# Kernel optimization log

Hardware: AMD Instinct MI355X
Metric: run time of the kernel (lower is better)

## Reference

```python
import jax, jax.numpy as jnp
import numpy as np

B, S, D, H = 4, 1024, 1024, 16
DH = D // H  # head dim = 64
PAD = -1e7   # padding_num in source
EPS = 1e-3   # keras LayerNormalization default epsilon


def setup_inputs() -> dict:
    key = jax.random.key(0)
    ks = jax.random.split(key, 8)
    return {
        "queries": jax.random.normal(ks[0], (B, S, D), jnp.float32),
        "keys": jax.random.normal(ks[1], (B, S, D), jnp.float32),
        "values": jax.random.normal(ks[2], (B, S, D), jnp.float32),
        "query_masks": jax.random.randint(ks[3], (B, S), 0, 2, jnp.int32),
        "key_masks": jax.random.randint(ks[4], (B, S), 0, 2, jnp.int32),
        "Wq": jax.random.normal(ks[5], (D, D), jnp.float32) * (D ** -0.5),
        "Wk": jax.random.normal(ks[6], (D, D), jnp.float32) * (D ** -0.5),
        "Wv": jax.random.normal(ks[7], (D, D), jnp.float32) * (D ** -0.5),
        "gamma": jnp.ones((D,), jnp.float32),
        "beta": jnp.zeros((D,), jnp.float32),
    }


def reference(queries, keys, values, query_masks, key_masks, Wq, Wk, Wv, gamma, beta):
    # QKV projections (no bias)
    Q = queries @ Wq  # [B,S,D]
    K = keys @ Wk
    V = values @ Wv
    # split heads: tf.split(axis=2)+concat(axis=0) == head-major layout [H,B,S,DH]
    Qh = Q.reshape(B, S, H, DH).transpose(2, 0, 1, 3)
    Kh = K.reshape(B, S, H, DH).transpose(2, 0, 1, 3)
    Vh = V.reshape(B, S, H, DH).transpose(2, 0, 1, 3)
    # scaled scores; note source scales by head_dim ** 0.5 (d_k of split K)
    scores = jnp.einsum("hbqd,hbkd->hbqk", Qh, Kh) / (DH ** 0.5)
    # additive key mask: positions where key_mask==0 get large negative
    scores = jnp.where(key_masks[None, :, None, :] == 0, PAD, scores)
    attn = jax.nn.softmax(scores, axis=-1)
    # multiplicative query mask AFTER softmax (as in source)
    attn = attn * query_masks[None, :, :, None].astype(jnp.float32)
    out = jnp.einsum("hbqk,hbkd->hbqd", attn, Vh)  # [H,B,S,DH]
    # merge heads back: concat over feature axis in head order
    out = out.transpose(1, 2, 0, 3).reshape(B, S, D)
    # residual + LayerNorm
    res = queries + out
    mean = jnp.mean(res, axis=-1, keepdims=True)
    var = jnp.mean(jnp.square(res - mean), axis=-1, keepdims=True)
    return gamma * (res - mean) * jax.lax.rsqrt(var + EPS) + beta
```

## Files before the change

### kernel.cpp

```cpp
#include <hip/hip_runtime.h>

#define BB   4
#define SS   1024
#define DD   1024
#define HH   16
#define DHH  64
#define LN_EPS  (1e-3f)

typedef unsigned short u16;
typedef __attribute__((ext_vector_type(8))) short bf16x8;
typedef __attribute__((ext_vector_type(4))) float f32x4;

__device__ __forceinline__ u16 f2bf(float f) {
    union { float f; unsigned int u; } v; v.f = f;
    return (u16)((v.u + 0x7FFFu + ((v.u >> 16) & 1u)) >> 16);
}

__device__ __forceinline__ unsigned int cvt_pk_bf16(float lo, float hi) {
    unsigned int r;
    asm("v_cvt_pk_bf16_f32 %0, %1, %2" : "=v"(r) : "v"(lo), "v"(hi));
    return r;
}

__device__ __forceinline__ void cp16(void* lds, const void* g) {
    __builtin_amdgcn_global_load_lds(
        (const __attribute__((address_space(1))) unsigned int*)g,
        (__attribute__((address_space(3))) unsigned int*)lds, 16, 0, 0);
}

__global__ __launch_bounds__(256) void prep(const float* __restrict__ q,
                                            const float* __restrict__ k,
                                            const float* __restrict__ v,
                                            const float* __restrict__ Wq,
                                            const float* __restrict__ Wk,
                                            const float* __restrict__ Wv,
                                            u16* __restrict__ Abf,
                                            u16* __restrict__ WtA) {
    __shared__ float Ts[64][65];
    const int z = blockIdx.z;
    const int tid = threadIdx.x;
    if (z < 3) {
        const float* src = (z == 0) ? q : (z == 1) ? k : v;
        u16* dst = Abf + (size_t)z * ((size_t)BB * SS * DD);
        const int N8 = BB * SS * DD / 8;
        for (int i = blockIdx.x * 256 + tid; i < N8; i += 256 * 256) {
            const float4 f0 = ((const float4*)src)[i * 2];
            const float4 f1 = ((const float4*)src)[i * 2 + 1];
            union { u16 u[8]; uint4 o; } t;
            t.u[0] = f2bf(f0.x); t.u[1] = f2bf(f0.y);
            t.u[2] = f2bf(f0.z); t.u[3] = f2bf(f0.w);
            t.u[4] = f2bf(f1.x); t.u[5] = f2bf(f1.y);
            t.u[6] = f2bf(f1.z); t.u[7] = f2bf(f1.w);
            ((uint4*)dst)[i] = t.o;
        }
    } else {
        const float* W = (z == 3) ? Wq : (z == 4) ? Wk : Wv;
        u16* Wt = WtA + (size_t)(z - 3) * DD * DD;
        const int k0 = (blockIdx.x >> 4) * 64, n0 = (blockIdx.x & 15) * 64;
        #pragma unroll
        for (int it = 0; it < 4; ++it) {
            const int idx = tid + it * 256;
            const int r = idx >> 4, c4 = (idx & 15) * 4;
            const float4 vv = *(const float4*)&W[(size_t)(k0 + r) * DD + n0 + c4];
            Ts[r][c4 + 0] = vv.x; Ts[r][c4 + 1] = vv.y;
            Ts[r][c4 + 2] = vv.z; Ts[r][c4 + 3] = vv.w;
        }
        __syncthreads();
        const int n = tid >> 2, kc = (tid & 3) * 16;
        #pragma unroll
        for (int p = 0; p < 8; ++p) {
            const unsigned int lo = f2bf(Ts[kc + p * 2 + 0][n]);
            const unsigned int hi = f2bf(Ts[kc + p * 2 + 1][n]);
            *(unsigned int*)&Wt[(size_t)(n0 + n) * DD + k0 + kc + p * 2] = lo | (hi << 16);
        }
    }
}

__global__ __launch_bounds__(512, 2) void gemm_fused(const u16* __restrict__ Abf,
                                                     const u16* __restrict__ WtA,
                                                     u16* __restrict__ Qbf,
                                                     u16* __restrict__ Kbf,
                                                     u16* __restrict__ Vtb) {
    __shared__ u16 lds[2][2][2][8192];

    const int bid = blockIdx.x;
    const int swz = (bid & 7) * 24 + (bid >> 3);
    const int z   = swz >> 6;
    const int rem = swz & 63;
    const int m0  = (rem >> 2) * 256;
    const int n0  = (rem & 3) * 256;

    const u16* A  = Abf + (size_t)z * ((size_t)BB * SS * DD);
    const u16* Bm = WtA + (size_t)z * (DD * DD);

    const int tid  = threadIdx.x;
    const int wave = tid >> 6, lane = tid & 63;
    const int ln = lane & 15, quad = lane >> 4;
    const int wr = wave >> 2, wc = wave & 3;

    int r_[2], c_[2];
    #pragma unroll
    for (int rd = 0; rd < 2; ++rd) {
        const int l = rd * 512 + tid;
        const int rr = l >> 2, cs = l & 3;
        r_[rd] = rr;
        c_[rd] = cs ^ ((rr >> 1) & 3);
    }
    const u16* srcA[2] = { A  + (size_t)(m0 + r_[0]) * DD + c_[0] * 8,
                           A  + (size_t)(m0 + r_[1]) * DD + c_[1] * 8 };
    const u16* srcB[2] = { Bm + (size_t)(n0 + r_[0]) * DD + c_[0] * 8,
                           Bm + (size_t)(n0 + r_[1]) * DD + c_[1] * 8 };

    int offA[8], offB[4];
    #pragma unroll
    for (int mi = 0; mi < 8; ++mi) {
        const int r = wr * 128 + mi * 16 + ln;
        offA[mi] = (r * 4 + (quad ^ ((r >> 1) & 3))) * 8;
    }
    #pragma unroll
    for (int nj = 0; nj < 4; ++nj) {
        const int r = wc * 64 + nj * 16 + ln;
        offB[nj] = (r * 4 + (quad ^ ((r >> 1) & 3))) * 8;
    }

    auto stage = [&](int T, int x) {
        const int cb = T & 1;
        const int koff = T * 64 + x * 32;
        #pragma unroll
        for (int rd = 0; rd < 2; ++rd) {
            cp16(&lds[cb][x][0][(rd * 512 + wave * 64) * 8], srcA[rd] + koff);
            cp16(&lds[cb][x][1][(rd * 512 + wave * 64) * 8], srcB[rd] + koff);
        }
    };

    f32x4 acc[8][4] = {};

    stage(0, 0); stage(0, 1); stage(1, 0);
    asm volatile("s_waitcnt vmcnt(8)" ::: "memory");
    __builtin_amdgcn_s_barrier();

    #pragma unroll
    for (int t = 0; t < 16; ++t) {
        const int c = t & 1;
        #pragma unroll
        for (int x = 0; x < 2; ++x) {
            if (x == 0) { if (t < 15) stage(t + 1, 1); }
            else        { if (t < 14) stage(t + 2, 0); }

            bf16x8 af[8], bfv[4];
            const u16* Ar = &lds[c][x][0][0];
            const u16* Br = &lds[c][x][1][0];
            #pragma unroll
            for (int mi = 0; mi < 8; ++mi) af[mi] = *(const bf16x8*)&Ar[offA[mi]];
            #pragma unroll
            for (int nj = 0; nj < 4; ++nj) bfv[nj] = *(const bf16x8*)&Br[offB[nj]];

            if (x == 0) {
                if (t < 15) asm volatile("s_waitcnt vmcnt(8)" ::: "memory");
                else        asm volatile("s_waitcnt vmcnt(0)" ::: "memory");
            } else {
                if (t < 14)       asm volatile("s_waitcnt vmcnt(8)" ::: "memory");
                else if (t == 14) asm volatile("s_waitcnt vmcnt(4)" ::: "memory");
            }
            __builtin_amdgcn_s_barrier();

            __builtin_amdgcn_s_setprio(1);
            #pragma unroll
            for (int mi = 0; mi < 8; ++mi)
                #pragma unroll
                for (int nj = 0; nj < 4; ++nj)
                    acc[mi][nj] = __builtin_amdgcn_mfma_f32_16x16x32_bf16(
                        af[mi], bfv[nj], acc[mi][nj], 0, 0, 0);
            __builtin_amdgcn_s_setprio(0);
            __builtin_amdgcn_s_barrier();
        }
    }

    const int hh = (n0 >> 6) + wc;
    if (z < 2) {
        u16* C = (z == 0) ? Qbf : Kbf;
        const float scale = (z == 0) ? 0.18033688f : 1.0f;
        #pragma unroll
        for (int mi = 0; mi < 8; ++mi) {
            const int mbase = m0 + wr * 128 + mi * 16 + quad * 4;
            const int bb = mbase >> 10, sb = mbase & 1023;
            #pragma unroll
            for (int nj = 0; nj < 4; ++nj) {
                const int dh = nj * 16 + ln;
                #pragma unroll
                for (int r = 0; r < 4; ++r)
                    C[(((size_t)bb * HH + hh) * SS + sb + r) * DHH + dh] =
                        f2bf(acc[mi][nj][r] * scale);
            }
        }
    } else {
        #pragma unroll
        for (int mi = 0; mi < 8; ++mi) {
            const int mbase = m0 + wr * 128 + mi * 16 + quad * 4;
            const int bb = mbase >> 10, sb = mbase & 1023;
            #pragma unroll
            for (int nj = 0; nj < 4; ++nj) {
                const int dh = nj * 16 + ln;
                uint2 pk;
                pk.x = cvt_pk_bf16(acc[mi][nj][0], acc[mi][nj][1]);
                pk.y = cvt_pk_bf16(acc[mi][nj][2], acc[mi][nj][3]);
                *(uint2*)&Vtb[(((size_t)bb * HH + hh) * DHH + dh) * SS + sb] = pk;
            }
        }
    }
}

__global__ __launch_bounds__(512) void attn_mfma(const u16* __restrict__ Qg,
                                                 const u16* __restrict__ Kg,
                                                 const u16* __restrict__ Vtg,
                                                 const int* __restrict__ qmask,
                                                 const int* __restrict__ kmask,
                                                 float* __restrict__ O) {
    __shared__ u16 Ps[128 * 68];
    __shared__ u16 Ks[2][64 * 64];
    __shared__ u16 Vs[2][64 * 64];
    __shared__ float kmLds[SS];

    const int bid  = blockIdx.x;
    const int xcd  = bid & 7;
    const int rest = bid >> 3;
    const int bh   = (rest & 7) * 8 + xcd;
    const int qt   = rest >> 3;
    const int b    = bh >> 4, h = bh & 15;
    const int q0   = qt * 128;
    const int tid  = threadIdx.x;
    const int wave = tid >> 6, lane = tid & 63;
    const int ln = lane & 15, quad = lane >> 4;
    const size_t bhs = (size_t)b * HH + h;

    const int sr = tid >> 3, scsrc = (tid & 7) ^ ((tid >> 3) & 7);
    const u16* kSrc = &Kg[(bhs * SS + sr) * DHH + scsrc * 8];
    const u16* vSrc = &Vtg[(bhs * DHH + sr) * SS + scsrc * 8];
    auto stageKV = [&](int t) {
        const int cb = t & 1;
        cp16(&Ks[cb][wave * 512], kSrc + (size_t)t * 64 * DHH);
        cp16(&Vs[cb][wave * 512], vSrc + t * 64);
    };

    const u16* qrow = &Qg[(bhs * SS + q0 + wave * 16 + ln) * DHH];
    const bf16x8 qf0 = *(const bf16x8*)&qrow[quad * 8];
    const bf16x8 qf1 = *(const bf16x8*)&qrow[32 + quad * 8];
    asm volatile("" ::: "memory");
    if (wave < 4)
        cp16(&kmLds[wave * 256], &kmask[b * SS + (wave * 64 + lane) * 4]);
    stageKV(0);
    stageKV(1);
    asm volatile("s_waitcnt vmcnt(2)" ::: "memory");
    __builtin_amdgcn_s_barrier();

    {
        const int2 iv = *(const int2*)&kmLds[tid * 2];
        float2 fv; fv.x = (float)iv.x; fv.y = (float)iv.y;
        *(float2*)&kmLds[tid * 2] = fv;
    }
    asm volatile("s_waitcnt lgkmcnt(0)" ::: "memory");
    __builtin_amdgcn_s_barrier();

    int off[4][2];
    #pragma unroll
    for (int nt = 0; nt < 4; ++nt) {
        const int r = nt * 16 + ln;
        off[nt][0] = ((r << 3) + ((0 + quad) ^ (r & 7))) << 3;
        off[nt][1] = ((r << 3) + ((4 + quad) ^ (r & 7))) << 3;
    }

    f32x4 o[4] = {};
    float lsum = 0.f;
    const f32x4 zero = {0.f, 0.f, 0.f, 0.f};
    const int prow = (wave * 16 + ln) * 68;

    #pragma unroll 2
    for (int kt = 0; kt < SS / 64; ++kt) {
        const int cb = kt & 1;
        const u16* Kc = Ks[cb];
        const u16* Vc = Vs[cb];

        #pragma unroll
        for (int nt = 0; nt < 4; ++nt) {
            const bf16x8 k0f = *(const bf16x8*)&Kc[off[nt][0]];
            const bf16x8 k1f = *(const bf16x8*)&Kc[off[nt][1]];
            f32x4 sacc = __builtin_amdgcn_mfma_f32_16x16x32_bf16(k0f, qf0, zero, 0, 0, 0);
            sacc = __builtin_amdgcn_mfma_f32_16x16x32_bf16(k1f, qf1, sacc, 0, 0, 0);
            const float4 fm = *(const float4*)&kmLds[kt * 64 + nt * 16 + quad * 4];
            const float p0 = fm.x * __builtin_amdgcn_exp2f(sacc[0]);
            const float p1 = fm.y * __builtin_amdgcn_exp2f(sacc[1]);
            const float p2 = fm.z * __builtin_amdgcn_exp2f(sacc[2]);
            const float p3 = fm.w * __builtin_amdgcn_exp2f(sacc[3]);
            lsum += (p0 + p1) + (p2 + p3);
            uint2 pk;
            pk.x = cvt_pk_bf16(p0, p1);
            pk.y = cvt_pk_bf16(p2, p3);
            *(uint2*)&Ps[prow + nt * 16 + quad * 4] = pk;
        }

        __builtin_amdgcn_s_setprio(1);
        #pragma unroll
        for (int kk2 = 0; kk2 < 2; ++kk2) {
            const bf16x8 pf = *(const bf16x8*)&Ps[prow + kk2 * 32 + quad * 8];
            #pragma unroll
            for (int nt2 = 0; nt2 < 4; ++nt2) {
                const bf16x8 vf = *(const bf16x8*)&Vc[off[nt2][kk2]];
                o[nt2] = __builtin_amdgcn_mfma_f32_16x16x32_bf16(pf, vf, o[nt2], 0, 0, 0);
            }
        }
        __builtin_amdgcn_s_setprio(0);

        if (kt == SS / 64 - 1) break;
        __builtin_amdgcn_s_barrier();
        if (kt + 2 < SS / 64) {
            stageKV(kt + 2);
            asm volatile("s_waitcnt vmcnt(2)" ::: "memory");
        } else {
            asm volatile("s_waitcnt vmcnt(0)" ::: "memory");
        }
        __builtin_amdgcn_s_barrier();
    }

    lsum += __shfl_xor(lsum, 16);
    lsum += __shfl_xor(lsum, 32);
    #pragma unroll
    for (int r = 0; r < 4; ++r) {
        const int qloc = quad * 4 + r;
        const float l = __shfl(lsum, qloc);
        const int q = q0 + wave * 16 + qloc;
        const float scale = (float)qmask[b * SS + q] / l;
        #pragma unroll
        for (int nt2 = 0; nt2 < 4; ++nt2)
            O[((size_t)b * SS + q) * DD + h * DHH + nt2 * 16 + ln] = o[nt2][r] * scale;
    }
}

__global__ __launch_bounds__(256) void ln_kernel(const float* __restrict__ Qin,
                                                 const float* __restrict__ attn,
                                                 const float* __restrict__ gamma,
                                                 const float* __restrict__ beta,
                                                 float* __restrict__ out) {
    const int row = blockIdx.x;
    const int tid = threadIdx.x;
    const int wid = tid >> 6, lane = tid & 63;
    __shared__ float sred[4];

    const float4 qv = ((const float4*)Qin)[(size_t)row * 256 + tid];
    const float4 av = ((const float4*)attn)[(size_t)row * 256 + tid];
    float4 v;
    v.x = qv.x + av.x; v.y = qv.y + av.y;
    v.z = qv.z + av.z; v.w = qv.w + av.w;

    float sum = v.x + v.y + v.z + v.w;
    #pragma unroll
    for (int off = 32; off; off >>= 1) sum += __shfl_down(sum, off);
    if (lane == 0) sred[wid] = sum;
    __syncthreads();
    const float mean = (sred[0] + sred[1] + sred[2] + sred[3]) * (1.0f / DD);
    __syncthreads();

    const float dx = v.x - mean, dy = v.y - mean, dz = v.z - mean, dw = v.w - mean;
    float vs = dx * dx + dy * dy + dz * dz + dw * dw;
    #pragma unroll
    for (int off = 32; off; off >>= 1) vs += __shfl_down(vs, off);
    if (lane == 0) sred[wid] = vs;
    __syncthreads();
    const float var = (sred[0] + sred[1] + sred[2] + sred[3]) * (1.0f / DD);
    const float inv = rsqrtf(var + LN_EPS);

    const float4 g = ((const float4*)gamma)[tid];
    const float4 bt = ((const float4*)beta)[tid];
    float4 ov;
    ov.x = g.x * dx * inv + bt.x; ov.y = g.y * dy * inv + bt.y;
    ov.z = g.z * dz * inv + bt.z; ov.w = g.w * dw * inv + bt.w;
    ((float4*)out)[(size_t)row * 256 + tid] = ov;
}

extern "C" void kernel_launch(void* const* d_in, const int* in_sizes, int n_in,
                              void* d_out, int out_size, void* d_ws, size_t ws_size,
                              hipStream_t stream) {
    const float* queries = (const float*)d_in[0];
    const float* keys    = (const float*)d_in[1];
    const float* values  = (const float*)d_in[2];
    const int*   qmask   = (const int*)d_in[3];
    const int*   kmask   = (const int*)d_in[4];
    const float* Wq      = (const float*)d_in[5];
    const float* Wk      = (const float*)d_in[6];
    const float* Wv      = (const float*)d_in[7];
    const float* gamma   = (const float*)d_in[8];
    const float* beta    = (const float*)d_in[9];
    float* out = (float*)d_out;

    const size_t NTOK = (size_t)BB * SS;
    u16* Abf = (u16*)d_ws;
    float* Ob = (float*)d_ws;
    u16* Qbf = Abf + 3 * NTOK * DD;
    u16* Kbf = Qbf + NTOK * DD;
    u16* Vtb = Kbf + NTOK * DD;
    u16* WtA = Vtb + NTOK * DD;

    prep<<<dim3(256, 1, 6), 256, 0, stream>>>(queries, keys, values, Wq, Wk, Wv, Abf, WtA);

    gemm_fused<<<192, 512, 0, stream>>>(Abf, WtA, Qbf, Kbf, Vtb);

    attn_mfma<<<BB * HH * (SS / 128), 512, 0, stream>>>(Qbf, Kbf, Vtb, qmask, kmask, Ob);

    ln_kernel<<<BB * SS, 256, 0, stream>>>(queries, Ob, gamma, beta, out);
}
```

Baseline: 186.9 us.

## Shrink QKV GEMM tiles to 128x128 with 256-thread blocks and simpler pipeline

Result: no change. 185.2 us (-0.9%).

```diff
diff --git a/kernel.cpp b/kernel.cpp
--- a/kernel.cpp
+++ b/kernel.cpp
@@ -76,19 +76,20 @@
     }
 }
 
-__global__ __launch_bounds__(512, 2) void gemm_fused(const u16* __restrict__ Abf,
-                                                     const u16* __restrict__ WtA,
-                                                     u16* __restrict__ Qbf,
-                                                     u16* __restrict__ Kbf,
-                                                     u16* __restrict__ Vtb) {
-    __shared__ u16 lds[2][2][2][8192];
+__global__ __launch_bounds__(256) void gemm_fused(const u16* __restrict__ Abf,
+                                                  const u16* __restrict__ WtA,
+                                                  u16* __restrict__ Qbf,
+                                                  u16* __restrict__ Kbf,
+                                                  u16* __restrict__ Vtb) {
+    __shared__ u16 As[2][128 * 64];
+    __shared__ u16 Bs[2][128 * 64];
 
     const int bid = blockIdx.x;
-    const int swz = (bid & 7) * 24 + (bid >> 3);
-    const int z   = swz >> 6;
-    const int rem = swz & 63;
-    const int m0  = (rem >> 2) * 256;
-    const int n0  = (rem & 3) * 256;
+    const int swz = (bid & 7) * 96 + (bid >> 3);
+    const int z   = swz >> 8;
+    const int rem = swz & 255;
+    const int m0  = (rem >> 3) * 128;
+    const int n0  = (rem & 7) * 128;
 
     const u16* A  = Abf + (size_t)z * ((size_t)BB * SS * DD);
     const u16* Bm = WtA + (size_t)z * (DD * DD);
@@ -96,114 +97,94 @@
     const int tid  = threadIdx.x;
     const int wave = tid >> 6, lane = tid & 63;
     const int ln = lane & 15, quad = lane >> 4;
-    const int wr = wave >> 2, wc = wave & 3;
-
-    int r_[2], c_[2];
-    #pragma unroll
-    for (int rd = 0; rd < 2; ++rd) {
-        const int l = rd * 512 + tid;
-        const int rr = l >> 2, cs = l & 3;
-        r_[rd] = rr;
-        c_[rd] = cs ^ ((rr >> 1) & 3);
-    }
-    const u16* srcA[2] = { A  + (size_t)(m0 + r_[0]) * DD + c_[0] * 8,
-                           A  + (size_t)(m0 + r_[1]) * DD + c_[1] * 8 };
-    const u16* srcB[2] = { Bm + (size_t)(n0 + r_[0]) * DD + c_[0] * 8,
-                           Bm + (size_t)(n0 + r_[1]) * DD + c_[1] * 8 };
-
-    int offA[8], offB[4];
-    #pragma unroll
-    for (int mi = 0; mi < 8; ++mi) {
-        const int r = wr * 128 + mi * 16 + ln;
-        offA[mi] = (r * 4 + (quad ^ ((r >> 1) & 3))) * 8;
-    }
-    #pragma unroll
-    for (int nj = 0; nj < 4; ++nj) {
-        const int r = wc * 64 + nj * 16 + ln;
-        offB[nj] = (r * 4 + (quad ^ ((r >> 1) & 3))) * 8;
-    }
-
-    auto stage = [&](int T, int x) {
+    const int mw = (wave & 1) * 64, nw = (wave >> 1) * 64;
+
+    const u16* srcA[4];
+    const u16* srcB[4];
+    #pragma unroll
+    for (int w = 0; w < 4; ++w) {
+        const int l = w * 256 + tid;
+        const int r = l >> 3, cs = l & 7;
+        const int c = cs ^ (r & 7);
+        srcA[w] = A  + (size_t)(m0 + r) * DD + c * 8;
+        srcB[w] = Bm + (size_t)(n0 + r) * DD + c * 8;
+    }
+
+    auto stage = [&](int T) {
         const int cb = T & 1;
-        const int koff = T * 64 + x * 32;
-        #pragma unroll
-        for (int rd = 0; rd < 2; ++rd) {
-            cp16(&lds[cb][x][0][(rd * 512 + wave * 64) * 8], srcA[rd] + koff);
-            cp16(&lds[cb][x][1][(rd * 512 + wave * 64) * 8], srcB[rd] + koff);
-        }
+        const int koff = T * 64;
+        #pragma unroll
+        for (int w = 0; w < 4; ++w)
+            cp16(&As[cb][(w * 256 + wave * 64) * 8], srcA[w] + koff);
+        #pragma unroll
+        for (int w = 0; w < 4; ++w)
+            cp16(&Bs[cb][(w * 256 + wave * 64) * 8], srcB[w] + koff);
     };
 
-    f32x4 acc[8][4] = {};
-
-    stage(0, 0); stage(0, 1); stage(1, 0);
-    asm volatile("s_waitcnt vmcnt(8)" ::: "memory");
-    __builtin_amdgcn_s_barrier();
-
+    f32x4 acc[4][4] = {};
+
+    stage(0);
     #pragma unroll
     for (int t = 0; t < 16; ++t) {
-        const int c = t & 1;
-        #pragma unroll
-        for (int x = 0; x < 2; ++x) {
-            if (x == 0) { if (t < 15) stage(t + 1, 1); }
-            else        { if (t < 14) stage(t + 2, 0); }
-
-            bf16x8 af[8], bfv[4];
-            const u16* Ar = &lds[c][x][0][0];
-            const u16* Br = &lds[c][x][1][0];
-            #pragma unroll
-            for (int mi = 0; mi < 8; ++mi) af[mi] = *(const bf16x8*)&Ar[offA[mi]];
-            #pragma unroll
-            for (int nj = 0; nj < 4; ++nj) bfv[nj] = *(const bf16x8*)&Br[offB[nj]];
-
-            if (x == 0) {
-                if (t < 15) asm volatile("s_waitcnt vmcnt(8)" ::: "memory");
-                else        asm volatile("s_waitcnt vmcnt(0)" ::: "memory");
-            } else {
-                if (t < 14)       asm volatile("s_waitcnt vmcnt(8)" ::: "memory");
-                else if (t == 14) asm volatile("s_waitcnt vmcnt(4)" ::: "memory");
-            }
-            __builtin_amdgcn_s_barrier();
-
+        const int cb = t & 1;
+        if (t < 15) stage(t + 1);
+        if (t < 15) asm volatile("s_waitcnt vmcnt(8)" ::: "memory");
+        else        asm volatile("s_waitcnt vmcnt(0)" ::: "memory");
+        __builtin_amdgcn_s_barrier();
+
+        #pragma unroll
+        for (int kk = 0; kk < 2; ++kk) {
+            bf16x8 af[4], bfv[4];
+            #pragma unroll
+            for (int i = 0; i < 4; ++i) {
+                const int r = mw + i * 16 + ln;
+                af[i] = *(const bf16x8*)&As[cb][((r << 3) + ((kk * 4 + quad) ^ (r & 7))) << 3];
+            }
+            #pragma unroll
+            for (int j = 0; j < 4; ++j) {
+                const int r = nw + j * 16 + ln;
+                bfv[j] = *(const bf16x8*)&Bs[cb][((r << 3) + ((kk * 4 + quad) ^ (r & 7))) << 3];
+            }
             __builtin_amdgcn_s_setprio(1);
             #pragma unroll
-            for (int mi = 0; mi < 8; ++mi)
+            for (int i = 0; i < 4; ++i)
                 #pragma unroll
-                for (int nj = 0; nj < 4; ++nj)
-                    acc[mi][nj] = __builtin_amdgcn_mfma_f32_16x16x32_bf16(
-                        af[mi], bfv[nj], acc[mi][nj], 0, 0, 0);
+                for (int j = 0; j < 4; ++j)
+                    acc[i][j] = __builtin_amdgcn_mfma_f32_16x16x32_bf16(af[i], bfv[j], acc[i][j], 0, 0, 0);
             __builtin_amdgcn_s_setprio(0);
-            __builtin_amdgcn_s_barrier();
-        }
-    }
-
-    const int hh = (n0 >> 6) + wc;
+        }
+        __builtin_amdgcn_s_barrier();
+    }
+
     if (z < 2) {
         u16* C = (z == 0) ? Qbf : Kbf;
         const float scale = (z == 0) ? 0.18033688f : 1.0f;
         #pragma unroll
-        for (int mi = 0; mi < 8; ++mi) {
-            const int mbase = m0 + wr * 128 + mi * 16 + quad * 4;
+        for (int i = 0; i < 4; ++i) {
+            const int mbase = m0 + mw + i * 16 + quad * 4;
             const int bb = mbase >> 10, sb = mbase & 1023;
             #pragma unroll
-            for (int nj = 0; nj < 4; ++nj) {
-                const int dh = nj * 16 + ln;
+            for (int j = 0; j < 4; ++j) {
+                const int n = n0 + nw + j * 16 + ln;
+                const int hh = n >> 6, dh = n & 63;
                 #pragma unroll
                 for (int r = 0; r < 4; ++r)
                     C[(((size_t)bb * HH + hh) * SS + sb + r) * DHH + dh] =
-                        f2bf(acc[mi][nj][r] * scale);
+                        f2bf(acc[i][j][r] * scale);
             }
         }
     } else {
         #pragma unroll
-        for (int mi = 0; mi < 8; ++mi) {
-            const int mbase = m0 + wr * 128 + mi * 16 + quad * 4;
+        for (int i = 0; i < 4; ++i) {
+            const int mbase = m0 + mw + i * 16 + quad * 4;
             const int bb = mbase >> 10, sb = mbase & 1023;
             #pragma unroll
-            for (int nj = 0; nj < 4; ++nj) {
-                const int dh = nj * 16 + ln;
+            for (int j = 0; j < 4; ++j) {
+                const int n = n0 + nw + j * 16 + ln;
+                const int hh = n >> 6, dh = n & 63;
                 uint2 pk;
-                pk.x = cvt_pk_bf16(acc[mi][nj][0], acc[mi][nj][1]);
-                pk.y = cvt_pk_bf16(acc[mi][nj][2], acc[mi][nj][3]);
+                pk.x = cvt_pk_bf16(acc[i][j][0], acc[i][j][1]);
+                pk.y = cvt_pk_bf16(acc[i][j][2], acc[i][j][3]);
                 *(uint2*)&Vtb[(((size_t)bb * HH + hh) * DHH + dh) * SS + sb] = pk;
             }
         }
@@ -401,7 +382,7 @@
 
     prep<<<dim3(256, 1, 6), 256, 0, stream>>>(queries, keys, values, Wq, Wk, Wv, Abf, WtA);
 
-    gemm_fused<<<192, 512, 0, stream>>>(Abf, WtA, Qbf, Kbf, Vtb);
+    gemm_fused<<<768, 256, 0, stream>>>(Abf, WtA, Qbf, Kbf, Vtb);
 
     attn_mfma<<<BB * HH * (SS / 128), 512, 0, stream>>>(Qbf, Kbf, Vtb, qmask, kmask, Ob);
 
```
